# Optimization experiments

Measured on AMD Instinct MI355X. Metric: run time of the kernel, lower is better.

Reference implementation:

```python
import jax, jax.numpy as jnp
import numpy as np

N_NODES = 100000
N_EDGES = 3200000
IN_DIM = 128
HID = 64
OUT_DIM = 128
N_GRAPHS = 8


def _gcn_conv(x, W, b, src, dst, w, n):
    # GCNConv (PyG default): add self-loops (weight 1), symmetric normalization
    loop = jnp.arange(n)
    src2 = jnp.concatenate([src, loop])
    dst2 = jnp.concatenate([dst, loop])
    w2 = jnp.concatenate([w, jnp.ones((n,), x.dtype)])
    deg = jax.ops.segment_sum(w2, dst2, num_segments=n)
    dinv = jnp.where(deg > 0, jax.lax.rsqrt(deg), 0.0)
    norm = dinv[src2] * w2 * dinv[dst2]            # [E+N]
    h = x @ W                                      # transform before gather
    msg = h[src2] * norm[:, None]                  # gather + scale
    out = jax.ops.segment_sum(msg, dst2, num_segments=n)  # scatter-add
    return out + b


def setup_inputs() -> dict:
    key = jax.random.key(0)
    ks = jax.random.split(key, 10)
    x = jax.random.normal(ks[0], (N_NODES, IN_DIM), dtype=jnp.float32)
    edge_index = jax.random.randint(ks[1], (2, N_EDGES), 0, N_NODES, dtype=jnp.int64)
    edge_weight = jax.random.uniform(ks[2], (N_EDGES,), dtype=jnp.float32)
    batch = jnp.sort(jax.random.randint(ks[3], (N_NODES,), 0, N_GRAPHS, dtype=jnp.int64))
    # params (glorot-ish scale)
    W1 = jax.random.normal(ks[4], (IN_DIM, HID), dtype=jnp.float32) / np.sqrt(IN_DIM)
    b1 = jnp.zeros((HID,), jnp.float32)
    W2 = jax.random.normal(ks[5], (HID, HID), dtype=jnp.float32) / np.sqrt(HID)
    b2 = jnp.zeros((HID,), jnp.float32)
    Wfc = jax.random.normal(ks[6], (HID, OUT_DIM), dtype=jnp.float32) / np.sqrt(HID)
    bfc = jnp.zeros((OUT_DIM,), jnp.float32)
    return {"x": x, "edge_index": edge_index, "edge_weight": edge_weight,
            "batch": batch, "W1": W1, "b1": b1, "W2": W2, "b2": b2,
            "Wfc": Wfc, "bfc": bfc}


def reference(x, edge_index, edge_weight, batch, W1, b1, W2, b2, Wfc, bfc):
    src, dst = edge_index[0], edge_index[1]
    n = x.shape[0]
    h = _gcn_conv(x, W1, b1, src, dst, edge_weight, n)
    h = jax.nn.relu(h)
    h = _gcn_conv(h, W2, b2, src, dst, edge_weight, n)
    # global_mean_pool over batch ids
    sums = jax.ops.segment_sum(h, batch, num_segments=N_GRAPHS)
    cnts = jax.ops.segment_sum(jnp.ones((n,), h.dtype), batch, num_segments=N_GRAPHS)
    pooled = sums / jnp.maximum(cnts, 1.0)[:, None]
    return pooled @ Wfc + bfc
```

## Files before the change

kernel.cpp:

```cpp
#include <hip/hip_runtime.h>

#define IN_DIM 128
#define HID 64
#define OUT_DIM 128
#define NGRAPH 8

#define CHUNK 4096
#define BSH 9
#define BSZ 512

typedef unsigned long long u64;
typedef unsigned int u32;
typedef __attribute__((ext_vector_type(8))) short short8;
typedef __attribute__((ext_vector_type(4))) float f32x4;

__device__ inline short bf16b(float f) {
    u32 u = __float_as_uint(f);
    return (short)((u + 0x7FFFu + ((u >> 16) & 1u)) >> 16);
}
__device__ inline u32 pack_bf16(float a, float b) {
    u32 ua = (__float_as_uint(a) + 0x8000u) >> 16;
    u32 ub = (__float_as_uint(b) + 0x8000u) & 0xFFFF0000u;
    return ua | ub;
}
__device__ inline float bf16_lo(u32 v) { return __uint_as_float(v << 16); }
__device__ inline float bf16_hi(u32 v) { return __uint_as_float(v & 0xFFFF0000u); }

__global__ __launch_bounds__(256) void bhist_kernel(const int* __restrict__ dst,
                                                    u32* __restrict__ hist,
                                                    int E, int nchunk, int nbuck) {
    __shared__ u32 h[256];
    h[threadIdx.x] = 0;
    __syncthreads();
    int c = blockIdx.x;
    int beg = c * CHUNK, end = min(beg + CHUNK, E);
    for (int i = beg + threadIdx.x; i < end; i += 256)
        atomicAdd(&h[dst[i] >> BSH], 1u);
    __syncthreads();
    for (int b = threadIdx.x; b < nbuck; b += 256)
        hist[(size_t)b * nchunk + c] = h[b];
}

__global__ __launch_bounds__(512) void scanS1(u32* __restrict__ hist, u32* __restrict__ tot,
                                              int nchunk, int nbuck) {
    __shared__ u32 sm[1024];
    int b = blockIdx.x;
    int i0 = threadIdx.x, i1 = threadIdx.x + 512;
    u32 v0 = (i0 < nchunk) ? hist[(size_t)b * nchunk + i0] : 0;
    u32 v1 = (i1 < nchunk) ? hist[(size_t)b * nchunk + i1] : 0;
    sm[i0] = v0; sm[i1] = v1;
    __syncthreads();
    for (int off = 1; off < 1024; off <<= 1) {
        u32 t0 = (i0 >= off) ? sm[i0 - off] : 0;
        u32 t1 = (i1 >= off) ? sm[i1 - off] : 0;
        __syncthreads();
        sm[i0] += t0; sm[i1] += t1;
        __syncthreads();
    }
    if (i0 < nchunk) hist[(size_t)b * nchunk + i0] = sm[i0] - v0;
    if (i1 < nchunk) hist[(size_t)b * nchunk + i1] = sm[i1] - v1;
    if (threadIdx.x == 511) tot[b] = sm[1023];
}

__global__ __launch_bounds__(512) void scanS2(const u32* __restrict__ tot, u32* __restrict__ base,
                                              int nbuck) {
    __shared__ u32 sm[512];
    u32 v = (threadIdx.x < nbuck) ? tot[threadIdx.x] : 0;
    sm[threadIdx.x] = v;
    __syncthreads();
    for (int off = 1; off < 512; off <<= 1) {
        u32 t = (threadIdx.x >= off) ? sm[threadIdx.x - off] : 0;
        __syncthreads();
        sm[threadIdx.x] += t;
        __syncthreads();
    }
    if ((int)threadIdx.x <= nbuck) base[threadIdx.x] = sm[threadIdx.x] - v;
}

__global__ __launch_bounds__(256) void bin_kernel(const int* __restrict__ src,
                                                  const int* __restrict__ dst,
                                                  const float* __restrict__ ew,
                                                  const u32* __restrict__ offs,
                                                  const u32* __restrict__ base,
                                                  int2* __restrict__ bse,
                                                  int E, int nchunk, int nbuck) {
    __shared__ u32 lcnt[256];
    __shared__ u32 lpos[256];
    __shared__ u32 gbase[256];
    __shared__ int2 buf[CHUNK];
    __shared__ unsigned char bb[CHUNK];

    int c = blockIdx.x;
    int beg = c * CHUNK, end = min(beg + CHUNK, E);
    lcnt[threadIdx.x] = 0;
    __syncthreads();
    for (int i = beg + threadIdx.x; i < end; i += 256)
        atomicAdd(&lcnt[dst[i] >> BSH], 1u);
    __syncthreads();
    u32 v = lcnt[threadIdx.x];
    lpos[threadIdx.x] = v;
    __syncthreads();
    for (int off = 1; off < 256; off <<= 1) {
        u32 t = (threadIdx.x >= off) ? lpos[threadIdx.x - off] : 0;
        __syncthreads();
        lpos[threadIdx.x] += t;
        __syncthreads();
    }
    u32 excl = lpos[threadIdx.x] - v;
    __syncthreads();
    lpos[threadIdx.x] = excl;
    lcnt[threadIdx.x] = excl;
    if (threadIdx.x < (u32)nbuck)
        gbase[threadIdx.x] = base[threadIdx.x] + offs[(size_t)threadIdx.x * nchunk + c];
    __syncthreads();
    for (int i = beg + threadIdx.x; i < end; i += 256) {
        int d = dst[i];
        int b = d >> BSH;
        u32 p = atomicAdd(&lcnt[b], 1u);
        buf[p] = make_int2(src[i] | ((d & (BSZ - 1)) << 17), __float_as_int(ew[i]));
        bb[p] = (unsigned char)b;
    }
    __syncthreads();
    int tot = end - beg;
    for (int j = threadIdx.x; j < tot; j += 256) {
        int b = bb[j];
        bse[gbase[b] + j - lpos[b]] = buf[j];
    }
}

__global__ __launch_bounds__(256) void csr_kernel(const int2* __restrict__ bse,
                                                  const u32* __restrict__ base,
                                                  int* __restrict__ row_ptr,
                                                  float* __restrict__ dinv,
                                                  int2* __restrict__ edges, int N) {
    __shared__ u32 cnt[BSZ];
    __shared__ float wdeg[BSZ];
    __shared__ u32 rp[BSZ];
    int b = blockIdx.x;
    int beg = base[b], end = base[b + 1];
    int i0 = threadIdx.x, i1 = threadIdx.x + 256;
    cnt[i0] = 0; cnt[i1] = 0; wdeg[i0] = 0.f; wdeg[i1] = 0.f;
    __syncthreads();
    for (int i = beg + threadIdx.x; i < end; i += 256) {
        int2 e = bse[i];
        int dl = (e.x >> 17) & (BSZ - 1);
        atomicAdd(&cnt[dl], 1u);
        atomicAdd(&wdeg[dl], __int_as_float(e.y));
    }
    __syncthreads();
    u32 v0 = cnt[i0], v1 = cnt[i1];
    rp[i0] = v0; rp[i1] = v1;
    __syncthreads();
    for (int off = 1; off < BSZ; off <<= 1) {
        u32 t0 = (i0 >= off) ? rp[i0 - off] : 0;
        u32 t1 = (i1 >= off) ? rp[i1 - off] : 0;
        __syncthreads();
        rp[i0] += t0; rp[i1] += t1;
        __syncthreads();
    }
    int node0 = b * BSZ + i0, node1 = b * BSZ + i1;
    if (node0 <= N) row_ptr[node0] = beg + (int)(rp[i0] - v0);
    if (node1 <= N) row_ptr[node1] = beg + (int)(rp[i1] - v1);
    if (node0 < N) dinv[node0] = rsqrtf(wdeg[i0] + 1.0f);
    if (node1 < N) dinv[node1] = rsqrtf(wdeg[i1] + 1.0f);
    __syncthreads();
    cnt[i0] = rp[i0] - v0;
    cnt[i1] = rp[i1] - v1;
    __syncthreads();
    for (int i = beg + threadIdx.x; i < end; i += 256) {
        int2 e = bse[i];
        int dl = (e.x >> 17) & (BSZ - 1);
        u32 r = atomicAdd(&cnt[dl], 1u);
        edges[beg + r] = make_int2(e.x & 0x1FFFF, e.y);
    }
}

__global__ __launch_bounds__(256) void gemm1_kernel(const float* __restrict__ x,
                                                    const float* __restrict__ W1,
                                                    const float* __restrict__ dinv,
                                                    u32* __restrict__ hb, int N) {
    int wave = threadIdx.x >> 6, lane = threadIdx.x & 63;
    int col = lane & 15, kg = lane >> 4;
    int rowbase = blockIdx.x * 64 + wave * 16;

    short8 bW[4][4];
#pragma unroll
    for (int ks = 0; ks < 4; ++ks)
#pragma unroll
        for (int nt = 0; nt < 4; ++nt) {
            const float* wp = W1 + (size_t)(ks * 32 + kg * 8) * HID + nt * 16 + col;
            short8 f;
#pragma unroll
            for (int j = 0; j < 8; ++j) f[j] = bf16b(wp[j * HID]);
            bW[ks][nt] = f;
        }

    f32x4 acc[4];
#pragma unroll
    for (int nt = 0; nt < 4; ++nt) acc[nt] = (f32x4){0.f, 0.f, 0.f, 0.f};

    int arow = rowbase + col;
    if (arow >= N) arow = N - 1;
    const float4* xr = reinterpret_cast<const float4*>(x + (size_t)arow * IN_DIM);
#pragma unroll
    for (int ks = 0; ks < 4; ++ks) {
        float4 xa = xr[ks * 8 + kg * 2];
        float4 xb = xr[ks * 8 + kg * 2 + 1];
        short8 a;
        a[0] = bf16b(xa.x); a[1] = bf16b(xa.y); a[2] = bf16b(xa.z); a[3] = bf16b(xa.w);
        a[4] = bf16b(xb.x); a[5] = bf16b(xb.y); a[6] = bf16b(xb.z); a[7] = bf16b(xb.w);
#pragma unroll
        for (int nt = 0; nt < 4; ++nt)
            acc[nt] = __builtin_amdgcn_mfma_f32_16x16x32_bf16(a, bW[ks][nt], acc[nt], 0, 0, 0);
    }

#pragma unroll
    for (int r = 0; r < 4; ++r) {
        int row = rowbase + kg * 4 + r;
        if (row < N) {
            float di = dinv[row];
            hb[(size_t)row * 32 + col]      = pack_bf16(acc[0][r] * di, acc[2][r] * di);
            hb[(size_t)row * 32 + col + 16] = pack_bf16(acc[1][r] * di, acc[3][r] * di);
        }
    }
}

__global__ void agg_kernel(const int* __restrict__ row_ptr, const int2* __restrict__ edges,
                           const float* __restrict__ dinv, const u32* __restrict__ hb,
                           u32* __restrict__ aggb, int N) {
    int gid = blockIdx.x * blockDim.x + threadIdx.x;
    int node = gid >> 6, lane = gid & 63;
    if (node >= N) return;
    int half = lane >> 5, l = lane & 31;
    int beg = row_ptr[node], end = row_ptr[node + 1];
    int mid = beg + ((end - beg + 1) >> 1);
    int lo = half ? mid : beg;
    int hi = half ? end : mid;
    float ax = 0.f, ay = 0.f;
    if (half == 0) {
        u32 hv = hb[(size_t)node * 32 + l];
        ax = bf16_lo(hv);
        ay = bf16_hi(hv);
    }
    int i = lo;
    for (; i + 8 <= hi; i += 8) {
        int2 e0 = edges[i+0], e1 = edges[i+1], e2 = edges[i+2], e3 = edges[i+3];
        int2 e4 = edges[i+4], e5 = edges[i+5], e6 = edges[i+6], e7 = edges[i+7];
        u32 h0 = hb[(size_t)e0.x * 32 + l], h1 = hb[(size_t)e1.x * 32 + l];
        u32 h2 = hb[(size_t)e2.x * 32 + l], h3 = hb[(size_t)e3.x * 32 + l];
        u32 h4 = hb[(size_t)e4.x * 32 + l], h5 = hb[(size_t)e5.x * 32 + l];
        u32 h6 = hb[(size_t)e6.x * 32 + l], h7 = hb[(size_t)e7.x * 32 + l];
        float c0 = __int_as_float(e0.y), c1 = __int_as_float(e1.y);
        float c2 = __int_as_float(e2.y), c3 = __int_as_float(e3.y);
        float c4 = __int_as_float(e4.y), c5 = __int_as_float(e5.y);
        float c6 = __int_as_float(e6.y), c7 = __int_as_float(e7.y);
        ax += c0 * bf16_lo(h0); ay += c0 * bf16_hi(h0);
        ax += c1 * bf16_lo(h1); ay += c1 * bf16_hi(h1);
        ax += c2 * bf16_lo(h2); ay += c2 * bf16_hi(h2);
        ax += c3 * bf16_lo(h3); ay += c3 * bf16_hi(h3);
        ax += c4 * bf16_lo(h4); ay += c4 * bf16_hi(h4);
        ax += c5 * bf16_lo(h5); ay += c5 * bf16_hi(h5);
        ax += c6 * bf16_lo(h6); ay += c6 * bf16_hi(h6);
        ax += c7 * bf16_lo(h7); ay += c7 * bf16_hi(h7);
    }
    if (i < hi) {
        int2 e[8];
#pragma unroll
        for (int k = 0; k < 8; ++k) {
            int j = i + k;
            e[k] = edges[j < hi ? j : i];
            if (j >= hi) e[k].y = 0;
        }
        u32 hh[8];
#pragma unroll
        for (int k = 0; k < 8; ++k) hh[k] = hb[(size_t)e[k].x * 32 + l];
#pragma unroll
        for (int k = 0; k < 8; ++k) {
            float c = __int_as_float(e[k].y);
            ax += c * bf16_lo(hh[k]);
            ay += c * bf16_hi(hh[k]);
        }
    }
    ax += __shfl_xor(ax, 32);
    ay += __shfl_xor(ay, 32);
    float di = dinv[node];
    if (lane < 32) aggb[(size_t)node * 32 + l] = pack_bf16(di * ax, di * ay);
}

__global__ __launch_bounds__(256) void gemm2_kernel(const u32* __restrict__ aggb,
                                                    const float* __restrict__ b1,
                                                    const float* __restrict__ W2,
                                                    const float* __restrict__ dinv,
                                                    u32* __restrict__ hb, int N) {
    int wave = threadIdx.x >> 6, lane = threadIdx.x & 63;
    int col = lane & 15, kg = lane >> 4;
    int rowbase = blockIdx.x * 64 + wave * 16;

    short8 bW[2][4];
#pragma unroll
    for (int ks = 0; ks < 2; ++ks)
#pragma unroll
        for (int nt = 0; nt < 4; ++nt) {
            const float* wp = W2 + (size_t)(ks * 32 + kg * 8) * HID + nt * 16 + col;
            short8 f;
#pragma unroll
            for (int j = 0; j < 8; ++j) f[j] = bf16b(wp[j * HID]);
            bW[ks][nt] = f;
        }

    f32x4 acc[4];
#pragma unroll
    for (int nt = 0; nt < 4; ++nt) acc[nt] = (f32x4){0.f, 0.f, 0.f, 0.f};

    int arow = rowbase + col;
    if (arow >= N) arow = N - 1;
    const u32* ar = aggb + (size_t)arow * 32 + kg * 8;
    u32 w[8];
#pragma unroll
    for (int j = 0; j < 8; ++j) w[j] = ar[j];
#pragma unroll
    for (int ks = 0; ks < 2; ++ks) {
        short8 a;
#pragma unroll
        for (int j = 0; j < 8; ++j) {
            float f = ks ? bf16_hi(w[j]) : bf16_lo(w[j]);
            a[j] = bf16b(fmaxf(f + b1[ks * 32 + kg * 8 + j], 0.f));
        }
#pragma unroll
        for (int nt = 0; nt < 4; ++nt)
            acc[nt] = __builtin_amdgcn_mfma_f32_16x16x32_bf16(a, bW[ks][nt], acc[nt], 0, 0, 0);
    }

#pragma unroll
    for (int r = 0; r < 4; ++r) {
        int row = rowbase + kg * 4 + r;
        if (row < N) {
            float di = dinv[row];
            hb[(size_t)row * 32 + col]      = pack_bf16(acc[0][r] * di, acc[2][r] * di);
            hb[(size_t)row * 32 + col + 16] = pack_bf16(acc[1][r] * di, acc[3][r] * di);
        }
    }
}

__global__ void pool_kernel(const u32* __restrict__ aggb, const int* __restrict__ batch,
                            float* __restrict__ pooled, float* __restrict__ cnt,
                            int N, int chunk) {
    int wid = (blockIdx.x * blockDim.x + threadIdx.x) >> 6;
    int lane = threadIdx.x & 63;
    int w = lane & 31, hi = lane >> 5;
    int feat = w + hi * 32;
    int start = wid * chunk;
    if (start >= N) return;
    int end = min(start + chunk, N);
    float acc = 0.f, fc = 0.f;
    int cur = batch[start];
    for (int n = start; n < end; ++n) {
        int g = batch[n];
        if (g != cur) {
            atomicAdd(&pooled[cur * HID + feat], acc);
            if (lane == 0) atomicAdd(&cnt[cur], fc);
            cur = g; acc = 0.f; fc = 0.f;
        }
        u32 hv = aggb[(size_t)n * 32 + w];
        acc += hi ? bf16_hi(hv) : bf16_lo(hv);
        fc += 1.f;
    }
    atomicAdd(&pooled[cur * HID + feat], acc);
    if (lane == 0) atomicAdd(&cnt[cur], fc);
}

__global__ void final_kernel(const float* __restrict__ pooled, const float* __restrict__ cnt,
                             const float* __restrict__ b2, const float* __restrict__ Wfc,
                             const float* __restrict__ bfc, float* __restrict__ out) {
    int idx = blockIdx.x * blockDim.x + threadIdx.x;
    if (idx >= NGRAPH * OUT_DIM) return;
    int g = idx >> 7, o = idx & 127;
    float inv = 1.0f / fmaxf(cnt[g], 1.0f);
    float acc = 0.f;
#pragma unroll
    for (int k = 0; k < HID; ++k)
        acc += (pooled[g * HID + k] * inv + b2[k]) * Wfc[k * OUT_DIM + o];
    out[idx] = acc + bfc[o];
}

extern "C" void kernel_launch(void* const* d_in, const int* in_sizes, int n_in,
                              void* d_out, int out_size, void* d_ws, size_t ws_size,
                              hipStream_t stream) {
    const float* x    = (const float*)d_in[0];
    const int*   ei   = (const int*)d_in[1];
    const float* ew   = (const float*)d_in[2];
    const int*   bat  = (const int*)d_in[3];
    const float* W1   = (const float*)d_in[4];
    const float* b1   = (const float*)d_in[5];
    const float* W2   = (const float*)d_in[6];
    const float* b2   = (const float*)d_in[7];
    const float* Wfc  = (const float*)d_in[8];
    const float* bfc  = (const float*)d_in[9];
    float* out = (float*)d_out;

    const int N = in_sizes[0] / IN_DIM;
    const int E = in_sizes[2];
    const int* src = ei;
    const int* dst = ei + E;

    const int nbuck  = (N + BSZ - 1) >> BSH;
    const int nchunk = (E + CHUNK - 1) / CHUNK;

    char* ws = (char*)d_ws;
    size_t off = 0;
    auto alloc = [&](size_t bytes) {
        char* p = ws + off;
        off += (bytes + 255) / 256 * 256;
        return p;
    };
    u32*   hist    = (u32*)  alloc((size_t)nbuck * nchunk * 4);
    u32*   tot     = (u32*)  alloc(512 * 4);
    u32*   base    = (u32*)  alloc(512 * 4);
    int*   row_ptr = (int*)  alloc((size_t)(N + 1) * 4);
    float* dinv    = (float*)alloc((size_t)N * 4);
    float* pooled  = (float*)alloc((NGRAPH * HID + NGRAPH) * 4);
    float* cnt     = pooled + NGRAPH * HID;
    int2*  bse     = (int2*) alloc((size_t)E * 8);
    int2*  edges   = (int2*) alloc((size_t)E * 8);
    u32*   hb      = (u32*)  alloc((size_t)N * 32 * 4);
    u32*   aggb    = (u32*)  alloc((size_t)N * 32 * 4);

    hipMemsetAsync(pooled, 0, (NGRAPH * HID + NGRAPH) * 4, stream);

    bhist_kernel<<<nchunk, 256, 0, stream>>>(dst, hist, E, nchunk, nbuck);
    scanS1<<<nbuck, 512, 0, stream>>>(hist, tot, nchunk, nbuck);
    scanS2<<<1, 512, 0, stream>>>(tot, base, nbuck);
    bin_kernel<<<nchunk, 256, 0, stream>>>(src, dst, ew, hist, base, bse, E, nchunk, nbuck);
    csr_kernel<<<nbuck, 256, 0, stream>>>(bse, base, row_ptr, dinv, edges, N);

    int gemmBlocks = (N + 63) / 64;
    int rowBlocks = (int)(((size_t)N * 64 + 255) / 256);

    gemm1_kernel<<<gemmBlocks, 256, 0, stream>>>(x, W1, dinv, hb, N);
    agg_kernel<<<rowBlocks, 256, 0, stream>>>(row_ptr, edges, dinv, hb, aggb, N);

    gemm2_kernel<<<gemmBlocks, 256, 0, stream>>>(aggb, b1, W2, dinv, hb, N);
    agg_kernel<<<rowBlocks, 256, 0, stream>>>(row_ptr, edges, dinv, hb, aggb, N);

    const int POOL_WAVES = 1024;
    int chunk = (N + POOL_WAVES - 1) / POOL_WAVES;
    pool_kernel<<<POOL_WAVES / 4, 256, 0, stream>>>(aggb, bat, pooled, cnt, N, chunk);

    final_kernel<<<(NGRAPH * OUT_DIM + 255) / 256, 256, 0, stream>>>(pooled, cnt, b2, Wfc, bfc, out);
}
```

Before: 301.6 us.

## Shrink CSR destination buckets to 128 nodes and use fixed-point degree atomics

Bucket size drops from 512 to 128 nodes, so there are about 782 buckets instead of 196. This gives the scan and CSR stages roughly four times more blocks, which should improve occupancy across the GPU's CUs. The binning kernel's local scan is reworked to handle more than 256 buckets with per-thread segments, and the global bucket scan now runs on 1024 threads. Weighted degree accumulation switches from float shared atomics to integer fixed-point atomics (scaled by 2^20). This adds quantization error to the degree and risks overflow for very heavy nodes.

```diff
diff --git a/kernel.cpp b/kernel.cpp
--- a/kernel.cpp
+++ b/kernel.cpp
@@ -6,8 +6,9 @@
 #define NGRAPH 8
 
 #define CHUNK 4096
-#define BSH 9
-#define BSZ 512
+#define BSH 7
+#define BSZ 128
+#define MAXB 800
 
 typedef unsigned long long u64;
 typedef unsigned int u32;
@@ -29,8 +30,8 @@
 __global__ __launch_bounds__(256) void bhist_kernel(const int* __restrict__ dst,
                                                     u32* __restrict__ hist,
                                                     int E, int nchunk, int nbuck) {
-    __shared__ u32 h[256];
-    h[threadIdx.x] = 0;
+    __shared__ u32 h[MAXB];
+    for (int i = threadIdx.x; i < nbuck; i += 256) h[i] = 0;
     __syncthreads();
     int c = blockIdx.x;
     int beg = c * CHUNK, end = min(beg + CHUNK, E);
@@ -62,19 +63,23 @@
     if (threadIdx.x == 511) tot[b] = sm[1023];
 }
 
-__global__ __launch_bounds__(512) void scanS2(const u32* __restrict__ tot, u32* __restrict__ base,
-                                              int nbuck) {
-    __shared__ u32 sm[512];
-    u32 v = (threadIdx.x < nbuck) ? tot[threadIdx.x] : 0;
-    sm[threadIdx.x] = v;
-    __syncthreads();
-    for (int off = 1; off < 512; off <<= 1) {
-        u32 t = (threadIdx.x >= off) ? sm[threadIdx.x - off] : 0;
-        __syncthreads();
-        sm[threadIdx.x] += t;
-        __syncthreads();
-    }
-    if ((int)threadIdx.x <= nbuck) base[threadIdx.x] = sm[threadIdx.x] - v;
+__global__ __launch_bounds__(1024) void scanS2(const u32* __restrict__ tot,
+                                               u32* __restrict__ base, int nbuck) {
+    __shared__ u32 sm[2048];
+    int i0 = threadIdx.x, i1 = threadIdx.x + 1024;
+    u32 v0 = (i0 < nbuck) ? tot[i0] : 0;
+    u32 v1 = (i1 < nbuck) ? tot[i1] : 0;
+    sm[i0] = v0; sm[i1] = v1;
+    __syncthreads();
+    for (int off = 1; off < 2048; off <<= 1) {
+        u32 t0 = (i0 >= off) ? sm[i0 - off] : 0;
+        u32 t1 = (i1 >= off) ? sm[i1 - off] : 0;
+        __syncthreads();
+        sm[i0] += t0; sm[i1] += t1;
+        __syncthreads();
+    }
+    if (i0 <= nbuck) base[i0] = sm[i0] - v0;
+    if (i1 <= nbuck) base[i1] = sm[i1] - v1;
 }
 
 __global__ __launch_bounds__(256) void bin_kernel(const int* __restrict__ src,
@@ -84,45 +89,56 @@
                                                   const u32* __restrict__ base,
                                                   int2* __restrict__ bse,
                                                   int E, int nchunk, int nbuck) {
-    __shared__ u32 lcnt[256];
-    __shared__ u32 lpos[256];
-    __shared__ u32 gbase[256];
+    __shared__ u32 lcnt[MAXB];
+    __shared__ u32 lpos[MAXB];
+    __shared__ u32 gbase[MAXB];
+    __shared__ u32 part[256];
     __shared__ int2 buf[CHUNK];
-    __shared__ unsigned char bb[CHUNK];
+    __shared__ unsigned short bb[CHUNK];
 
     int c = blockIdx.x;
+    int tid = threadIdx.x;
     int beg = c * CHUNK, end = min(beg + CHUNK, E);
-    lcnt[threadIdx.x] = 0;
-    __syncthreads();
-    for (int i = beg + threadIdx.x; i < end; i += 256)
+    for (int b = tid; b < nbuck; b += 256) lcnt[b] = 0;
+    __syncthreads();
+    for (int i = beg + tid; i < end; i += 256)
         atomicAdd(&lcnt[dst[i] >> BSH], 1u);
     __syncthreads();
-    u32 v = lcnt[threadIdx.x];
-    lpos[threadIdx.x] = v;
+    int SEG = (nbuck + 255) >> 8;
+    u32 s = 0;
+    for (int j = 0; j < SEG; ++j) {
+        int b = tid * SEG + j;
+        if (b < nbuck) s += lcnt[b];
+    }
+    part[tid] = s;
     __syncthreads();
     for (int off = 1; off < 256; off <<= 1) {
-        u32 t = (threadIdx.x >= off) ? lpos[threadIdx.x - off] : 0;
-        __syncthreads();
-        lpos[threadIdx.x] += t;
-        __syncthreads();
-    }
-    u32 excl = lpos[threadIdx.x] - v;
-    __syncthreads();
-    lpos[threadIdx.x] = excl;
-    lcnt[threadIdx.x] = excl;
-    if (threadIdx.x < (u32)nbuck)
-        gbase[threadIdx.x] = base[threadIdx.x] + offs[(size_t)threadIdx.x * nchunk + c];
-    __syncthreads();
-    for (int i = beg + threadIdx.x; i < end; i += 256) {
+        u32 t = (tid >= off) ? part[tid - off] : 0;
+        __syncthreads();
+        part[tid] += t;
+        __syncthreads();
+    }
+    u32 run = part[tid] - s;
+    for (int j = 0; j < SEG; ++j) {
+        int b = tid * SEG + j;
+        if (b < nbuck) { u32 cv = lcnt[b]; lpos[b] = run; run += cv; }
+    }
+    __syncthreads();
+    for (int b = tid; b < nbuck; b += 256) {
+        lcnt[b] = lpos[b];
+        gbase[b] = base[b] + offs[(size_t)b * nchunk + c];
+    }
+    __syncthreads();
+    for (int i = beg + tid; i < end; i += 256) {
         int d = dst[i];
         int b = d >> BSH;
         u32 p = atomicAdd(&lcnt[b], 1u);
         buf[p] = make_int2(src[i] | ((d & (BSZ - 1)) << 17), __float_as_int(ew[i]));
-        bb[p] = (unsigned char)b;
+        bb[p] = (unsigned short)b;
     }
     __syncthreads();
     int tot = end - beg;
-    for (int j = threadIdx.x; j < tot; j += 256) {
+    for (int j = tid; j < tot; j += 256) {
         int b = bb[j];
         bse[gbase[b] + j - lpos[b]] = buf[j];
     }
@@ -134,40 +150,41 @@
                                                   float* __restrict__ dinv,
                                                   int2* __restrict__ edges, int N) {
     __shared__ u32 cnt[BSZ];
-    __shared__ float wdeg[BSZ];
+    __shared__ u32 wd[BSZ];
     __shared__ u32 rp[BSZ];
     int b = blockIdx.x;
+    int tid = threadIdx.x;
     int beg = base[b], end = base[b + 1];
-    int i0 = threadIdx.x, i1 = threadIdx.x + 256;
-    cnt[i0] = 0; cnt[i1] = 0; wdeg[i0] = 0.f; wdeg[i1] = 0.f;
-    __syncthreads();
-    for (int i = beg + threadIdx.x; i < end; i += 256) {
+    if (tid < BSZ) { cnt[tid] = 0; wd[tid] = 0; }
+    __syncthreads();
+    for (int i = beg + tid; i < end; i += 256) {
         int2 e = bse[i];
         int dl = (e.x >> 17) & (BSZ - 1);
         atomicAdd(&cnt[dl], 1u);
-        atomicAdd(&wdeg[dl], __int_as_float(e.y));
-    }
-    __syncthreads();
-    u32 v0 = cnt[i0], v1 = cnt[i1];
-    rp[i0] = v0; rp[i1] = v1;
+        atomicAdd(&wd[dl], (u32)__float2int_rn(__int_as_float(e.y) * 1048576.0f));
+    }
+    __syncthreads();
+    u32 v = 0;
+    if (tid < BSZ) { v = cnt[tid]; rp[tid] = v; }
     __syncthreads();
     for (int off = 1; off < BSZ; off <<= 1) {
-        u32 t0 = (i0 >= off) ? rp[i0 - off] : 0;
-        u32 t1 = (i1 >= off) ? rp[i1 - off] : 0;
-        __syncthreads();
-        rp[i0] += t0; rp[i1] += t1;
-        __syncthreads();
-    }
-    int node0 = b * BSZ + i0, node1 = b * BSZ + i1;
-    if (node0 <= N) row_ptr[node0] = beg + (int)(rp[i0] - v0);
-    if (node1 <= N) row_ptr[node1] = beg + (int)(rp[i1] - v1);
-    if (node0 < N) dinv[node0] = rsqrtf(wdeg[i0] + 1.0f);
-    if (node1 < N) dinv[node1] = rsqrtf(wdeg[i1] + 1.0f);
-    __syncthreads();
-    cnt[i0] = rp[i0] - v0;
-    cnt[i1] = rp[i1] - v1;
-    __syncthreads();
-    for (int i = beg + threadIdx.x; i < end; i += 256) {
+        u32 t = 0;
+        if (tid < BSZ && tid >= off) t = rp[tid - off];
+        __syncthreads();
+        if (tid < BSZ) rp[tid] += t;
+        __syncthreads();
+    }
+    if (tid < BSZ) {
+        int node = b * BSZ + tid;
+        u32 excl = rp[tid] - v;
+        if (node <= N) row_ptr[node] = beg + (int)excl;
+        if (node < N)
+            dinv[node] = rsqrtf((float)wd[tid] * (1.0f / 1048576.0f) + 1.0f);
+    }
+    __syncthreads();
+    if (tid < BSZ) cnt[tid] = rp[tid] - v;
+    __syncthreads();
+    for (int i = beg + tid; i < end; i += 256) {
         int2 e = bse[i];
         int dl = (e.x >> 17) & (BSZ - 1);
         u32 r = atomicAdd(&cnt[dl], 1u);
@@ -414,8 +431,8 @@
         return p;
     };
     u32*   hist    = (u32*)  alloc((size_t)nbuck * nchunk * 4);
-    u32*   tot     = (u32*)  alloc(512 * 4);
-    u32*   base    = (u32*)  alloc(512 * 4);
+    u32*   tot     = (u32*)  alloc(2048 * 4);
+    u32*   base    = (u32*)  alloc(2048 * 4);
     int*   row_ptr = (int*)  alloc((size_t)(N + 1) * 4);
     float* dinv    = (float*)alloc((size_t)N * 4);
     float* pooled  = (float*)alloc((NGRAPH * HID + NGRAPH) * 4);
@@ -429,7 +446,7 @@
 
     bhist_kernel<<<nchunk, 256, 0, stream>>>(dst, hist, E, nchunk, nbuck);
     scanS1<<<nbuck, 512, 0, stream>>>(hist, tot, nchunk, nbuck);
-    scanS2<<<1, 512, 0, stream>>>(tot, base, nbuck);
+    scanS2<<<1, 1024, 0, stream>>>(tot, base, nbuck);
     bin_kernel<<<nchunk, 256, 0, stream>>>(src, dst, ew, hist, base, bse, E, nchunk, nbuck);
     csr_kernel<<<nbuck, 256, 0, stream>>>(bse, base, row_ptr, dinv, edges, N);
 
```

New measurement: 306.7 us (median of 2 runs). Within noise of the previous version (+1.7%).
